# Performance work log

Measured on AMD Instinct MI355X. Metric: run time of the kernel, lower is better.

## Reference

```python
import jax, jax.numpy as jnp
import numpy as np
import math

B, S, HID = 2, 2048, 512
H, HKV, QB, VB = 8, 2, 8, 16
W = 256 // QB            # suffix window size = 32
QKD = W * QB             # unfolded qk dim = 256
TAU = 1.0


def setup_inputs() -> dict:
    key = jax.random.key(0)
    ks = jax.random.split(key, 7)
    return {
        "hidden_states": jax.random.normal(ks[0], (B, S, HID), jnp.float32),
        "Wq": jax.random.normal(ks[1], (H * QB, HID), jnp.float32) * (HID ** -0.5),
        "Wk": jax.random.normal(ks[2], (HKV * QB, HID), jnp.float32) * (HID ** -0.5),
        "Wv": jax.random.normal(ks[3], (HKV * VB, HID), jnp.float32) * (HID ** -0.5),
        "Wo": jax.random.normal(ks[4], (HID, H * VB), jnp.float32) * ((H * VB) ** -0.5),
        "v_emb0": jnp.full((H * VB,), -1e-5, jnp.float32),
        "v_emb1": jnp.full((H * VB,), +1e-5, jnp.float32),
    }


def _forward(hidden_states, Wq, Wk, Wv, Wo, v_emb0, v_emb1):
    b, s, _ = hidden_states.shape
    # bit-quantized (soft) q/k/v projections
    q = jnp.tanh((hidden_states @ Wq.T) / TAU).reshape(b, s, H, QB).transpose(0, 2, 1, 3)      # [B,H,S,QB]
    k = jnp.tanh((hidden_states @ Wk.T) / TAU).reshape(b, s, HKV, QB).transpose(0, 2, 1, 3)    # [B,HKV,S,QB]
    v = jax.nn.sigmoid((hidden_states @ Wv.T) / TAU).reshape(b, s, HKV, VB).transpose(0, 2, 1, 3)
    # suffix shift of values: F.pad(v, (0,0,-1,1)) -> v[t] <- v[t+1], last position zero
    v = jnp.concatenate([v[:, :, 1:], jnp.zeros_like(v[:, :, :1])], axis=2)                    # [B,HKV,S,VB]
    # left-pad seq by W-1 zeros, then unfold sliding windows of length W
    pad = ((0, 0), (0, 0), (W - 1, 0), (0, 0))
    qp, kp = jnp.pad(q, pad), jnp.pad(k, pad)
    win = jnp.arange(s)[:, None] + jnp.arange(W)[None, :]   # [S,W] window indices into padded seq
    qw = qp[:, :, win, :].reshape(b, H, s, QKD)             # concat window positions x bits
    kw = kp[:, :, win, :].reshape(b, HKV, s, QKD)
    # GQA: repeat kv heads
    rep = H // HKV
    kw = jnp.repeat(kw, rep, axis=1)
    vr = jnp.repeat(v, rep, axis=1)
    scale = 1.0 / math.sqrt(QKD) / TAU
    # custom bias r_j / (r_i + 1) under strictly-causal mask (j < i)
    r = jnp.arange(s, dtype=hidden_states.dtype)
    mask = jnp.tril(jnp.ones((s, s), dtype=bool), -1)
    bias = jnp.where(mask, (r[None, :] / (r[:, None] + 1.0)) / TAU, 0.0)
    scores = jnp.einsum('bhqd,bhkd->bhqk', qw, kw) * scale + bias
    neg = jnp.finfo(scores.dtype).min
    scores = jnp.where(mask, scores, neg)
    # stable masked softmax (fully-masked row 0 -> zero weights instead of NaN)
    scores = scores - jax.lax.stop_gradient(jnp.max(scores, axis=-1, keepdims=True))
    e = jnp.exp(scores) * mask
    attn = e / jnp.maximum(jnp.sum(e, axis=-1, keepdims=True), 1e-30)
    out = jnp.einsum('bhqk,bhkd->bhqd', attn, vr)           # [B,H,S,VB]
    out = out.transpose(0, 2, 1, 3).reshape(b, s, H * VB)
    # learned emb0/emb1 interpolation
    out = out * v_emb1 + (1.0 - out) * v_emb0
    return out @ Wo.T


def reference(hidden_states, Wq, Wk, Wv, Wo, v_emb0, v_emb1):
    return _forward(hidden_states, Wq, Wk, Wv, Wo, v_emb0, v_emb1)
```

## Files before the change

### kernel.cpp

```cpp
#include <hip/hip_runtime.h>
#include <hip/hip_bf16.h>

typedef unsigned int u32;
typedef unsigned short u16;
typedef float f32x4 __attribute__((ext_vector_type(4)));
typedef short s16x8 __attribute__((ext_vector_type(8)));
typedef u32 u32x2 __attribute__((ext_vector_type(2)));

#define B_   2
#define S_   2048
#define HID_ 512
#define H_   8
#define HKV_ 2
#define QB_  8
#define VB_  16
#define NQ_  64
#define NC_  112
#define HVB_ 128
#define SCALE_ 0.0625f
#define MFIX_  17.0f

__device__ __forceinline__ u16 f2bf(float f) {
    u32 b = __builtin_bit_cast(u32, f);
    b += 0x7FFFu + ((b >> 16) & 1u);
    return (u16)(b >> 16);
}
__device__ __forceinline__ float bf2f(u16 h) {
    u32 b = ((u32)h) << 16;
    return __builtin_bit_cast(float, b);
}
__device__ __forceinline__ f32x4 mfma16(s16x8 a, s16x8 b, f32x4 c) {
    return __builtin_amdgcn_mfma_f32_16x16x32_bf16(a, b, c, 0, 0, 0);
}
__device__ __forceinline__ float fast_tanh(float x) {
    float e = __expf(2.f * x);
    return 1.f - 2.f * __builtin_amdgcn_rcpf(e + 1.f);
}
__device__ __forceinline__ float fast_sigmoid(float x) {
    return __builtin_amdgcn_rcpf(1.f + __expf(-x));
}

__global__ void k0_convert(const float* __restrict__ Wq, const float* __restrict__ Wk,
                           const float* __restrict__ Wv, const float* __restrict__ Wo,
                           u16* __restrict__ W2c_hi, u16* __restrict__ W2c_lo,
                           u16* __restrict__ W2o_hi, u16* __restrict__ W2o_lo) {
    int idx = blockIdx.x * 256 + threadIdx.x;
    if (idx < NC_ * HID_) {
        int n = idx >> 9, k = idx & 511;
        float v = (n < NQ_) ? Wq[n * HID_ + k]
                : (n < NQ_ + 16) ? Wk[(n - NQ_) * HID_ + k]
                : Wv[(n - NQ_ - 16) * HID_ + k];
        int dst = ((k >> 5) * NC_ + n) * 32 + (k & 31);
        u16 hi = f2bf(v);
        W2c_hi[dst] = hi;
        W2c_lo[dst] = f2bf(v - bf2f(hi));
    }
    if (idx < HID_ * HVB_) {
        int o = idx >> 7, k = idx & 127;
        float v = Wo[idx];
        int dst = ((k >> 5) * HID_ + o) * 32 + (k & 31);
        u16 hi = f2bf(v);
        W2o_hi[dst] = hi;
        W2o_lo[dst] = f2bf(v - bf2f(hi));
    }
}

__global__ __launch_bounds__(256) void k1_proj(
    const float* __restrict__ hidden,
    const u16* __restrict__ W2c_hi, const u16* __restrict__ W2c_lo,
    u16* __restrict__ qb, u16* __restrict__ kb, u16* __restrict__ vt)
{
    __shared__ __align__(16) u32 Ahi[16 * 256];
    __shared__ __align__(16) u32 Alo[16 * 256];
    char* AhiB = (char*)Ahi;
    char* AloB = (char*)Alo;
    const int tid = threadIdx.x;
    const int r0 = blockIdx.x * 16;

    #pragma unroll
    for (int it = 0; it < 8; ++it) {
        int v4 = it * 256 + tid;
        int m = v4 >> 7, c4 = v4 & 127;
        f32x4 x = *(const f32x4*)&hidden[(r0 + m) * HID_ + 4 * c4];
        u16 h0 = f2bf(x[0]), h1 = f2bf(x[1]), h2 = f2bf(x[2]), h3 = f2bf(x[3]);
        u16 l0 = f2bf(x[0] - bf2f(h0)), l1 = f2bf(x[1] - bf2f(h1));
        u16 l2 = f2bf(x[2] - bf2f(h2)), l3 = f2bf(x[3] - bf2f(h3));
        int byt = (c4 * 8) ^ ((m & 7) << 4);
        *(u32x2*)(AhiB + m * 1024 + byt) = (u32x2){(u32)h0 | ((u32)h1 << 16), (u32)h2 | ((u32)h3 << 16)};
        *(u32x2*)(AloB + m * 1024 + byt) = (u32x2){(u32)l0 | ((u32)l1 << 16), (u32)l2 | ((u32)l3 << 16)};
    }
    __syncthreads();

    const int wv = tid >> 6, lane = tid & 63;
    const int li = lane & 15, lo4 = lane >> 4;
    const int nf = (wv == 3) ? 1 : 2;
    const int fl[2] = {wv, wv + 4};

    f32x4 acc[2];
    acc[0] = (f32x4){0.f, 0.f, 0.f, 0.f};
    acc[1] = (f32x4){0.f, 0.f, 0.f, 0.f};

    for (int kc = 0; kc < 16; ++kc) {
        int off = (64 * kc + 16 * lo4) ^ ((li & 7) << 4);
        s16x8 ah = *(const s16x8*)(AhiB + li * 1024 + off);
        s16x8 al = *(const s16x8*)(AloB + li * 1024 + off);
        #pragma unroll
        for (int u = 0; u < 2; ++u) {
            if (u < nf) {
                int n = fl[u] * 16 + li;
                int bidx = (kc * NC_ + n) * 32 + 8 * lo4;
                s16x8 bh = *(const s16x8*)&W2c_hi[bidx];
                s16x8 bl = *(const s16x8*)&W2c_lo[bidx];
                acc[u] = mfma16(ah, bh, acc[u]);
                acc[u] = mfma16(ah, bl, acc[u]);
                acc[u] = mfma16(al, bh, acc[u]);
            }
        }
    }

    #pragma unroll
    for (int u = 0; u < 2; ++u) {
        if (u < nf) {
            int n = fl[u] * 16 + li;
            #pragma unroll
            for (int reg = 0; reg < 4; ++reg) {
                int gs = r0 + 4 * lo4 + reg;
                int b = gs >> 11, s = gs & 2047;
                float pre = acc[u][reg];
                if (n < NQ_) {
                    int h = n >> 3, bit = n & 7;
                    qb[(((b * H_ + h) * S_) + s) * QB_ + bit] = f2bf(fast_tanh(pre));
                } else if (n < NQ_ + 16) {
                    int nk = n - NQ_;
                    kb[(((b * HKV_ + (nk >> 3)) * S_) + s) * QB_ + (nk & 7)] = f2bf(fast_tanh(pre));
                } else {
                    int nv = n - NQ_ - 16;
                    int hv = nv >> 4, vb = nv & 15;
                    u16 sig = f2bf(fast_sigmoid(pre));
                    if (s > 0)
                        vt[((b * HKV_ + hv) * VB_ + vb) * S_ + (s - 1)] = sig;
                    if (s == S_ - 1)
                        vt[((b * HKV_ + hv) * VB_ + vb) * S_ + (S_ - 1)] = 0;
                }
            }
        }
    }
}

__global__ __launch_bounds__(512, 4) void k2_attn(
    const u16* __restrict__ qb, const u16* __restrict__ kb, const u16* __restrict__ vt,
    const float* __restrict__ vemb0, const float* __restrict__ vemb1,
    float* __restrict__ AO)
{
    __shared__ __align__(16) u16 ks[2][2][96 * 8];
    __shared__ __align__(16) u16 psa[8][16 * 72];
    __shared__ __align__(16) float Om[8][16][17];
    __shared__ float lv[8][16];

    const int tid = threadIdx.x;
    const int bid = blockIdx.x;
    const int rb = bid >> 4;
    const int r  = (rb < 16) ? (31 - rb) : (rb - 16);
    const int I0 = r * 64;
    const int nJ = r + 1;
    const int bh = bid & 15;
    const int b = bh >> 3, h = bh & 7, hkv = h >> 2;

    const int qhb = ((b * H_ + h) * S_) * QB_;
    const int khb = ((b * HKV_ + hkv) * S_) * QB_;
    const int vhb = ((b * HKV_ + hkv) * VB_) * S_;

    const int w = tid >> 6, lane = tid & 63;
    const int g = w >> 2, wr = w & 3;
    const int li = lane & 15, lo4 = lane >> 4;
    const int tloc = tid & 255;

    u16* psw = psa[w];

    s16x8 af[8];
    {
        const int gr0 = I0 - 31 + 16 * wr + li + lo4;
        const u16* qp = qb + qhb + gr0 * QB_;
        #pragma unroll
        for (int kk = 0; kk < 8; ++kk) {
            s16x8 v = {0, 0, 0, 0, 0, 0, 0, 0};
            if (gr0 + 4 * kk >= 0) v = *(const s16x8*)(qp + kk * 32);
            af[kk] = v;
        }
    }

    int iv[4];
    float binv[4];
    #pragma unroll
    for (int reg = 0; reg < 4; ++reg) {
        iv[reg] = I0 + 16 * wr + 4 * lo4 + reg;
        binv[reg] = 1.0f / (float)(iv[reg] + 1);
    }

    f32x4 O = (f32x4){0.f, 0.f, 0.f, 0.f};
    float lsum[4] = {0.f, 0.f, 0.f, 0.f};

    const u16* vtp = vt + vhb + li * S_ + 8 * lo4;

    if (g < nJ && tloc < 96) {
        int gr = 64 * g - 31 + tloc;
        s16x8 v = {0, 0, 0, 0, 0, 0, 0, 0};
        if (gr >= 0) v = *(const s16x8*)(kb + khb + gr * QB_);
        *(s16x8*)&ks[g][0][tloc * 8] = v;
    }
    __syncthreads();

    const int nT = (nJ + 1) >> 1;
    for (int t = 0; t < nT; ++t) {
        const int cb = t & 1;
        const int jt = 2 * t + g;

        const bool do_stage = ((jt + 2) < nJ) && (tloc < 96);
        s16x8 stg;
        if (do_stage)
            stg = *(const s16x8*)(kb + khb + (64 * (jt + 2) - 31 + tloc) * QB_);

        if (jt < nJ) {
            const u16* kbuf = &ks[g][cb][(li + lo4) * 8];
            f32x4 sacc[4];
            #pragma unroll
            for (int ns = 0; ns < 4; ++ns) sacc[ns] = (f32x4){0.f, 0.f, 0.f, 0.f};
            #pragma unroll
            for (int m = 0; m < 20; ++m) {
                s16x8 f = *(const s16x8*)(kbuf + 32 * m);
                #pragma unroll
                for (int kk = (m & 3); kk < 8; kk += 4) {
                    int ns = (m - kk) >> 2;
                    if (ns >= 0 && ns < 4)
                        sacc[ns] = mfma16(af[kk], f, sacc[ns]);
                }
            }
            const int J0 = jt * 64;
            int jv[4];
            #pragma unroll
            for (int ns = 0; ns < 4; ++ns) jv[ns] = J0 + 16 * ns + li;
            #pragma unroll
            for (int reg = 0; reg < 4; ++reg) {
                #pragma unroll
                for (int ns = 0; ns < 4; ++ns) {
                    float s = fmaf(sacc[ns][reg], SCALE_, (float)jv[ns] * binv[reg]);
                    float p = (jv[ns] < iv[reg]) ? __expf(s - MFIX_) : 0.0f;
                    lsum[reg] += p;
                    psw[(4 * lo4 + reg) * 72 + 16 * ns + li] = f2bf(p);
                }
            }
            #pragma unroll
            for (int kk2 = 0; kk2 < 2; ++kk2) {
                s16x8 pa = *(const s16x8*)&psw[li * 72 + 32 * kk2 + 8 * lo4];
                s16x8 pb = *(const s16x8*)(vtp + J0 + 32 * kk2);
                O = mfma16(pa, pb, O);
            }
        }

        if (do_stage)
            *(s16x8*)&ks[g][cb ^ 1][tloc * 8] = stg;

        __syncthreads();
    }

    #pragma unroll
    for (int reg = 0; reg < 4; ++reg) {
        float l = lsum[reg];
        l += __shfl_xor(l, 1);
        l += __shfl_xor(l, 2);
        l += __shfl_xor(l, 4);
        l += __shfl_xor(l, 8);
        Om[w][4 * lo4 + reg][li] = O[reg];
        if (li == 0) lv[w][4 * lo4 + reg] = l;
    }
    __syncthreads();

    if (g == 0) {
        const int hc = h * VB_ + li;
        const float e0 = vemb0[hc], e1 = vemb1[hc];
        #pragma unroll
        for (int reg = 0; reg < 4; ++reg) {
            const int row = 4 * lo4 + reg;
            float Oc = Om[w][row][li] + Om[w + 4][row][li];
            float lc = lv[w][row] + lv[w + 4][row];
            float o = Oc / fmaxf(lc, 1e-30f);
            const int s = I0 + 16 * wr + row;
            AO[(b * S_ + s) * HVB_ + hc] = e0 + o * (e1 - e0);
        }
    }
}

__global__ __launch_bounds__(256) void k3_out(
    const float* __restrict__ AO,
    const u16* __restrict__ W2o_hi, const u16* __restrict__ W2o_lo,
    float* __restrict__ out)
{
    __shared__ __align__(16) u32 Ahi[16 * 64];
    __shared__ __align__(16) u32 Alo[16 * 64];
    char* AhiB = (char*)Ahi;
    char* AloB = (char*)Alo;
    const int tid = threadIdx.x;
    const int r0 = blockIdx.x * 16;

    #pragma unroll
    for (int it = 0; it < 2; ++it) {
        int v4 = it * 256 + tid;
        int m = v4 >> 5, c4 = v4 & 31;
        f32x4 x = *(const f32x4*)&AO[(r0 + m) * HVB_ + 4 * c4];
        u16 h0 = f2bf(x[0]), h1 = f2bf(x[1]), h2 = f2bf(x[2]), h3 = f2bf(x[3]);
        u16 l0 = f2bf(x[0] - bf2f(h0)), l1 = f2bf(x[1] - bf2f(h1));
        u16 l2 = f2bf(x[2] - bf2f(h2)), l3 = f2bf(x[3] - bf2f(h3));
        int byt = (c4 * 8) ^ ((m & 7) << 4);
        *(u32x2*)(AhiB + m * 256 + byt) = (u32x2){(u32)h0 | ((u32)h1 << 16), (u32)h2 | ((u32)h3 << 16)};
        *(u32x2*)(AloB + m * 256 + byt) = (u32x2){(u32)l0 | ((u32)l1 << 16), (u32)l2 | ((u32)l3 << 16)};
    }
    __syncthreads();

    const int wv = tid >> 6, lane = tid & 63;
    const int li = lane & 15, lo4 = lane >> 4;

    f32x4 acc[8];
    #pragma unroll
    for (int f = 0; f < 8; ++f) acc[f] = (f32x4){0.f, 0.f, 0.f, 0.f};

    #pragma unroll
    for (int kc = 0; kc < 4; ++kc) {
        int off = (64 * kc + 16 * lo4) ^ ((li & 7) << 4);
        s16x8 ah = *(const s16x8*)(AhiB + li * 256 + off);
        s16x8 al = *(const s16x8*)(AloB + li * 256 + off);
        #pragma unroll
        for (int f = 0; f < 8; ++f) {
            int o = wv * 128 + f * 16 + li;
            int bidx = (kc * HID_ + o) * 32 + 8 * lo4;
            s16x8 bh = *(const s16x8*)&W2o_hi[bidx];
            s16x8 bl = *(const s16x8*)&W2o_lo[bidx];
            acc[f] = mfma16(ah, bh, acc[f]);
            acc[f] = mfma16(ah, bl, acc[f]);
            acc[f] = mfma16(al, bh, acc[f]);
        }
    }

    #pragma unroll
    for (int f = 0; f < 8; ++f) {
        int o = wv * 128 + f * 16 + li;
        #pragma unroll
        for (int reg = 0; reg < 4; ++reg)
            out[(r0 + 4 * lo4 + reg) * HID_ + o] = acc[f][reg];
    }
}

extern "C" void kernel_launch(void* const* d_in, const int* in_sizes, int n_in,
                              void* d_out, int out_size, void* d_ws, size_t ws_size,
                              hipStream_t stream)
{
    (void)in_sizes; (void)n_in; (void)out_size;
    const float* hidden = (const float*)d_in[0];
    const float* Wq = (const float*)d_in[1];
    const float* Wk = (const float*)d_in[2];
    const float* Wv = (const float*)d_in[3];
    const float* Wo = (const float*)d_in[4];
    const float* ve0 = (const float*)d_in[5];
    const float* ve1 = (const float*)d_in[6];
    float* out = (float*)d_out;

    char* base = (char*)d_ws;
    u16* qb    = (u16*)(base);
    u16* kb    = (u16*)(base + 524288);
    u16* vt    = (u16*)(base + 655360);
    float* AO  = (float*)(base + 917504);
    u16* W2c_hi = (u16*)(base + 3014656);
    u16* W2c_lo = (u16*)(base + 3129344);
    u16* W2o_hi = (u16*)(base + 3244032);
    u16* W2o_lo = (u16*)(base + 3375104);
    if (ws_size < 3506176) return;

    hipLaunchKernelGGL(k0_convert, dim3(256), dim3(256), 0, stream,
                       Wq, Wk, Wv, Wo, W2c_hi, W2c_lo, W2o_hi, W2o_lo);
    hipLaunchKernelGGL(k1_proj, dim3(256), dim3(256), 0, stream,
                       hidden, W2c_hi, W2c_lo, qb, kb, vt);
    hipLaunchKernelGGL(k2_attn, dim3(512), dim3(512), 0, stream,
                       qb, kb, vt, ve0, ve1, AO);
    hipLaunchKernelGGL(k3_out, dim3(256), dim3(256), 0, stream,
                       AO, W2o_hi, W2o_lo, out);
}
```

Before: 63.66 us.

## Drop split-bf16 GEMMs, store AO as bf16, restructure attention to 256-thread blocks

```diff
diff --git a/kernel.cpp b/kernel.cpp
--- a/kernel.cpp
+++ b/kernel.cpp
@@ -5,7 +5,6 @@
 typedef unsigned short u16;
 typedef float f32x4 __attribute__((ext_vector_type(4)));
 typedef short s16x8 __attribute__((ext_vector_type(8)));
-typedef u32 u32x2 __attribute__((ext_vector_type(2)));
 
 #define B_   2
 #define S_   2048
@@ -15,7 +14,6 @@
 #define QB_  8
 #define VB_  16
 #define NQ_  64
-#define NC_  112
 #define HVB_ 128
 #define SCALE_ 0.0625f
 #define MFIX_  17.0f
@@ -42,86 +40,51 @@
 
 __global__ void k0_convert(const float* __restrict__ Wq, const float* __restrict__ Wk,
                            const float* __restrict__ Wv, const float* __restrict__ Wo,
-                           u16* __restrict__ W2c_hi, u16* __restrict__ W2c_lo,
-                           u16* __restrict__ W2o_hi, u16* __restrict__ W2o_lo) {
+                           u16* __restrict__ Wc, u16* __restrict__ Wob) {
     int idx = blockIdx.x * 256 + threadIdx.x;
-    if (idx < NC_ * HID_) {
+    {
         int n = idx >> 9, k = idx & 511;
         float v = (n < NQ_) ? Wq[n * HID_ + k]
                 : (n < NQ_ + 16) ? Wk[(n - NQ_) * HID_ + k]
-                : Wv[(n - NQ_ - 16) * HID_ + k];
-        int dst = ((k >> 5) * NC_ + n) * 32 + (k & 31);
-        u16 hi = f2bf(v);
-        W2c_hi[dst] = hi;
-        W2c_lo[dst] = f2bf(v - bf2f(hi));
-    }
-    if (idx < HID_ * HVB_) {
-        int o = idx >> 7, k = idx & 127;
-        float v = Wo[idx];
-        int dst = ((k >> 5) * HID_ + o) * 32 + (k & 31);
-        u16 hi = f2bf(v);
-        W2o_hi[dst] = hi;
-        W2o_lo[dst] = f2bf(v - bf2f(hi));
-    }
+                : (n < 112) ? Wv[(n - NQ_ - 16) * HID_ + k] : 0.f;
+        Wc[idx] = f2bf(v);
+    }
+    Wob[idx] = f2bf(Wo[idx]);
 }
 
 __global__ __launch_bounds__(256) void k1_proj(
-    const float* __restrict__ hidden,
-    const u16* __restrict__ W2c_hi, const u16* __restrict__ W2c_lo,
+    const float* __restrict__ hidden, const u16* __restrict__ Wc,
     u16* __restrict__ qb, u16* __restrict__ kb, u16* __restrict__ vt)
 {
-    __shared__ __align__(16) u32 Ahi[16 * 256];
-    __shared__ __align__(16) u32 Alo[16 * 256];
-    char* AhiB = (char*)Ahi;
-    char* AloB = (char*)Alo;
     const int tid = threadIdx.x;
     const int r0 = blockIdx.x * 16;
-
-    #pragma unroll
-    for (int it = 0; it < 8; ++it) {
-        int v4 = it * 256 + tid;
-        int m = v4 >> 7, c4 = v4 & 127;
-        f32x4 x = *(const f32x4*)&hidden[(r0 + m) * HID_ + 4 * c4];
-        u16 h0 = f2bf(x[0]), h1 = f2bf(x[1]), h2 = f2bf(x[2]), h3 = f2bf(x[3]);
-        u16 l0 = f2bf(x[0] - bf2f(h0)), l1 = f2bf(x[1] - bf2f(h1));
-        u16 l2 = f2bf(x[2] - bf2f(h2)), l3 = f2bf(x[3] - bf2f(h3));
-        int byt = (c4 * 8) ^ ((m & 7) << 4);
-        *(u32x2*)(AhiB + m * 1024 + byt) = (u32x2){(u32)h0 | ((u32)h1 << 16), (u32)h2 | ((u32)h3 << 16)};
-        *(u32x2*)(AloB + m * 1024 + byt) = (u32x2){(u32)l0 | ((u32)l1 << 16), (u32)l2 | ((u32)l3 << 16)};
-    }
-    __syncthreads();
-
     const int wv = tid >> 6, lane = tid & 63;
     const int li = lane & 15, lo4 = lane >> 4;
-    const int nf = (wv == 3) ? 1 : 2;
-    const int fl[2] = {wv, wv + 4};
+
+    const float* hrow = hidden + (r0 + li) * HID_;
 
     f32x4 acc[2];
     acc[0] = (f32x4){0.f, 0.f, 0.f, 0.f};
     acc[1] = (f32x4){0.f, 0.f, 0.f, 0.f};
 
+    #pragma unroll
     for (int kc = 0; kc < 16; ++kc) {
-        int off = (64 * kc + 16 * lo4) ^ ((li & 7) << 4);
-        s16x8 ah = *(const s16x8*)(AhiB + li * 1024 + off);
-        s16x8 al = *(const s16x8*)(AloB + li * 1024 + off);
+        f32x4 x0 = *(const f32x4*)&hrow[32 * kc + 8 * lo4];
+        f32x4 x1 = *(const f32x4*)&hrow[32 * kc + 8 * lo4 + 4];
+        s16x8 a = { (short)f2bf(x0[0]), (short)f2bf(x0[1]), (short)f2bf(x0[2]), (short)f2bf(x0[3]),
+                    (short)f2bf(x1[0]), (short)f2bf(x1[1]), (short)f2bf(x1[2]), (short)f2bf(x1[3]) };
         #pragma unroll
         for (int u = 0; u < 2; ++u) {
-            if (u < nf) {
-                int n = fl[u] * 16 + li;
-                int bidx = (kc * NC_ + n) * 32 + 8 * lo4;
-                s16x8 bh = *(const s16x8*)&W2c_hi[bidx];
-                s16x8 bl = *(const s16x8*)&W2c_lo[bidx];
-                acc[u] = mfma16(ah, bh, acc[u]);
-                acc[u] = mfma16(ah, bl, acc[u]);
-                acc[u] = mfma16(al, bh, acc[u]);
-            }
+            int n = (wv + 4 * u) * 16 + li;
+            s16x8 bfr = *(const s16x8*)&Wc[n * HID_ + 32 * kc + 8 * lo4];
+            acc[u] = mfma16(a, bfr, acc[u]);
         }
     }
 
     #pragma unroll
     for (int u = 0; u < 2; ++u) {
-        if (u < nf) {
-            int n = fl[u] * 16 + li;
+        int n = (wv + 4 * u) * 16 + li;
+        if (n < 112) {
             #pragma unroll
             for (int reg = 0; reg < 4; ++reg) {
                 int gs = r0 + 4 * lo4 + reg;
@@ -147,15 +110,15 @@
     }
 }
 
-__global__ __launch_bounds__(512, 4) void k2_attn(
+__global__ __launch_bounds__(256, 2) void k2_attn(
     const u16* __restrict__ qb, const u16* __restrict__ kb, const u16* __restrict__ vt,
     const float* __restrict__ vemb0, const float* __restrict__ vemb1,
-    float* __restrict__ AO)
+    u16* __restrict__ AO)
 {
     __shared__ __align__(16) u16 ks[2][2][96 * 8];
-    __shared__ __align__(16) u16 psa[8][16 * 72];
-    __shared__ __align__(16) float Om[8][16][17];
-    __shared__ float lv[8][16];
+    __shared__ __align__(16) u16 psa[4][32 * 72];
+    __shared__ __align__(16) float Om[4][2][16][17];
+    __shared__ float lv[4][2][16];
 
     const int tid = threadIdx.x;
     const int bid = blockIdx.x;
@@ -171,38 +134,43 @@
     const int vhb = ((b * HKV_ + hkv) * VB_) * S_;
 
     const int w = tid >> 6, lane = tid & 63;
-    const int g = w >> 2, wr = w & 3;
+    const int rw = w & 1, g = w >> 1;
     const int li = lane & 15, lo4 = lane >> 4;
-    const int tloc = tid & 255;
+    const int tloc = tid & 127;
 
     u16* psw = psa[w];
 
-    s16x8 af[8];
-    {
-        const int gr0 = I0 - 31 + 16 * wr + li + lo4;
+    s16x8 qf[2][8];
+    #pragma unroll
+    for (int ig = 0; ig < 2; ++ig) {
+        const int gr0 = I0 + 32 * rw + 16 * ig + li - 31 + lo4;
         const u16* qp = qb + qhb + gr0 * QB_;
         #pragma unroll
         for (int kk = 0; kk < 8; ++kk) {
             s16x8 v = {0, 0, 0, 0, 0, 0, 0, 0};
             if (gr0 + 4 * kk >= 0) v = *(const s16x8*)(qp + kk * 32);
-            af[kk] = v;
-        }
-    }
-
-    int iv[4];
-    float binv[4];
-    #pragma unroll
-    for (int reg = 0; reg < 4; ++reg) {
-        iv[reg] = I0 + 16 * wr + 4 * lo4 + reg;
-        binv[reg] = 1.0f / (float)(iv[reg] + 1);
-    }
-
-    f32x4 O = (f32x4){0.f, 0.f, 0.f, 0.f};
-    float lsum[4] = {0.f, 0.f, 0.f, 0.f};
+            qf[ig][kk] = v;
+        }
+    }
+
+    float binv[2][4];
+    #pragma unroll
+    for (int ig = 0; ig < 2; ++ig)
+        #pragma unroll
+        for (int reg = 0; reg < 4; ++reg) {
+            float d = (float)(I0 + 32 * rw + 16 * ig + 4 * lo4 + reg + 1);
+            float rc = __builtin_amdgcn_rcpf(d);
+            binv[ig][reg] = rc * (2.f - d * rc);
+        }
+
+    f32x4 O[2];
+    O[0] = (f32x4){0.f, 0.f, 0.f, 0.f};
+    O[1] = (f32x4){0.f, 0.f, 0.f, 0.f};
+    float lsum[2][4] = {{0.f, 0.f, 0.f, 0.f}, {0.f, 0.f, 0.f, 0.f}};
 
     const u16* vtp = vt + vhb + li * S_ + 8 * lo4;
 
-    if (g < nJ && tloc < 96) {
+    if (g < nJ && tloc < 95) {
         int gr = 64 * g - 31 + tloc;
         s16x8 v = {0, 0, 0, 0, 0, 0, 0, 0};
         if (gr >= 0) v = *(const s16x8*)(kb + khb + gr * QB_);
@@ -215,45 +183,66 @@
         const int cb = t & 1;
         const int jt = 2 * t + g;
 
-        const bool do_stage = ((jt + 2) < nJ) && (tloc < 96);
+        const bool do_stage = ((jt + 2) < nJ) && (tloc < 95);
         s16x8 stg;
         if (do_stage)
             stg = *(const s16x8*)(kb + khb + (64 * (jt + 2) - 31 + tloc) * QB_);
 
         if (jt < nJ) {
             const u16* kbuf = &ks[g][cb][(li + lo4) * 8];
-            f32x4 sacc[4];
-            #pragma unroll
-            for (int ns = 0; ns < 4; ++ns) sacc[ns] = (f32x4){0.f, 0.f, 0.f, 0.f};
+            f32x4 sacc[2][4];
+            #pragma unroll
+            for (int ig = 0; ig < 2; ++ig)
+                #pragma unroll
+                for (int ns = 0; ns < 4; ++ns)
+                    sacc[ig][ns] = (f32x4){0.f, 0.f, 0.f, 0.f};
             #pragma unroll
             for (int m = 0; m < 20; ++m) {
                 s16x8 f = *(const s16x8*)(kbuf + 32 * m);
-                #pragma unroll
-                for (int kk = (m & 3); kk < 8; kk += 4) {
-                    int ns = (m - kk) >> 2;
-                    if (ns >= 0 && ns < 4)
-                        sacc[ns] = mfma16(af[kk], f, sacc[ns]);
-                }
-            }
+                {
+                    int kk = m & 3, ns = m >> 2;
+                    if (ns < 4) {
+                        sacc[0][ns] = mfma16(qf[0][kk], f, sacc[0][ns]);
+                        sacc[1][ns] = mfma16(qf[1][kk], f, sacc[1][ns]);
+                    }
+                }
+                {
+                    int kk = (m & 3) + 4, ns = (m >> 2) - 1;
+                    if (ns >= 0) {
+                        sacc[0][ns] = mfma16(qf[0][kk], f, sacc[0][ns]);
+                        sacc[1][ns] = mfma16(qf[1][kk], f, sacc[1][ns]);
+                    }
+                }
+            }
+
             const int J0 = jt * 64;
             int jv[4];
             #pragma unroll
             for (int ns = 0; ns < 4; ++ns) jv[ns] = J0 + 16 * ns + li;
             #pragma unroll
-            for (int reg = 0; reg < 4; ++reg) {
+            for (int ig = 0; ig < 2; ++ig) {
                 #pragma unroll
-                for (int ns = 0; ns < 4; ++ns) {
-                    float s = fmaf(sacc[ns][reg], SCALE_, (float)jv[ns] * binv[reg]);
-                    float p = (jv[ns] < iv[reg]) ? __expf(s - MFIX_) : 0.0f;
-                    lsum[reg] += p;
-                    psw[(4 * lo4 + reg) * 72 + 16 * ns + li] = f2bf(p);
-                }
-            }
-            #pragma unroll
-            for (int kk2 = 0; kk2 < 2; ++kk2) {
-                s16x8 pa = *(const s16x8*)&psw[li * 72 + 32 * kk2 + 8 * lo4];
-                s16x8 pb = *(const s16x8*)(vtp + J0 + 32 * kk2);
-                O = mfma16(pa, pb, O);
+                for (int reg = 0; reg < 4; ++reg) {
+                    const int i = I0 + 32 * rw + 16 * ig + 4 * lo4 + reg;
+                    const float bi = binv[ig][reg];
+                    #pragma unroll
+                    for (int ns = 0; ns < 4; ++ns) {
+                        float s = fmaf(sacc[ig][ns][reg], SCALE_, (float)jv[ns] * bi);
+                        float p = (jv[ns] < i) ? __expf(s - MFIX_) : 0.0f;
+                        lsum[ig][reg] += p;
+                        psw[(ig * 16 + 4 * lo4 + reg) * 72 + 16 * ns + li] = f2bf(p);
+                    }
+                }
+            }
+
+            #pragma unroll
+            for (int ig = 0; ig < 2; ++ig) {
+                #pragma unroll
+                for (int kk2 = 0; kk2 < 2; ++kk2) {
+                    s16x8 pa = *(const s16x8*)&psw[(ig * 16 + li) * 72 + 32 * kk2 + 8 * lo4];
+                    s16x8 pb = *(const s16x8*)(vtp + J0 + 32 * kk2);
+                    O[ig] = mfma16(pa, pb, O[ig]);
+                }
             }
         }
 
@@ -264,14 +253,17 @@
     }
 
     #pragma unroll
-    for (int reg = 0; reg < 4; ++reg) {
-        float l = lsum[reg];
-        l += __shfl_xor(l, 1);
-        l += __shfl_xor(l, 2);
-        l += __shfl_xor(l, 4);
-        l += __shfl_xor(l, 8);
-        Om[w][4 * lo4 + reg][li] = O[reg];
-        if (li == 0) lv[w][4 * lo4 + reg] = l;
+    for (int ig = 0; ig < 2; ++ig) {
+        #pragma unroll
+        for (int reg = 0; reg < 4; ++reg) {
+            float l = lsum[ig][reg];
+            l += __shfl_xor(l, 1);
+            l += __shfl_xor(l, 2);
+            l += __shfl_xor(l, 4);
+            l += __shfl_xor(l, 8);
+            Om[w][ig][4 * lo4 + reg][li] = O[ig][reg];
+            if (li == 0) lv[w][ig][4 * lo4 + reg] = l;
+        }
     }
     __syncthreads();
 
@@ -279,73 +271,56 @@
         const int hc = h * VB_ + li;
         const float e0 = vemb0[hc], e1 = vemb1[hc];
         #pragma unroll
-        for (int reg = 0; reg < 4; ++reg) {
-            const int row = 4 * lo4 + reg;
-            float Oc = Om[w][row][li] + Om[w + 4][row][li];
-            float lc = lv[w][row] + lv[w + 4][row];
-            float o = Oc / fmaxf(lc, 1e-30f);
-            const int s = I0 + 16 * wr + row;
-            AO[(b * S_ + s) * HVB_ + hc] = e0 + o * (e1 - e0);
+        for (int ig = 0; ig < 2; ++ig) {
+            #pragma unroll
+            for (int reg = 0; reg < 4; ++reg) {
+                const int row = 4 * lo4 + reg;
+                float Oc = Om[w][ig][row][li] + Om[w + 2][ig][row][li];
+                float lc = lv[w][ig][row] + lv[w + 2][ig][row];
+                float lr = fmaxf(lc, 1e-30f);
+                float rinv = __builtin_amdgcn_rcpf(lr);
+                rinv = rinv * (2.f - lr * rinv);
+                float o = Oc * rinv;
+                const int s = I0 + 32 * rw + 16 * ig + row;
+                AO[(b * S_ + s) * HVB_ + hc] = f2bf(e0 + o * (e1 - e0));
+            }
         }
     }
 }
 
 __global__ __launch_bounds__(256) void k3_out(
-    const float* __restrict__ AO,
-    const u16* __restrict__ W2o_hi, const u16* __restrict__ W2o_lo,
+    const u16* __restrict__ AO, const u16* __restrict__ Wob,
     float* __restrict__ out)
 {
-    __shared__ __align__(16) u32 Ahi[16 * 64];
-    __shared__ __align__(16) u32 Alo[16 * 64];
-    char* AhiB = (char*)Ahi;
-    char* AloB = (char*)Alo;
     const int tid = threadIdx.x;
-    const int r0 = blockIdx.x * 16;
-
-    #pragma unroll
-    for (int it = 0; it < 2; ++it) {
-        int v4 = it * 256 + tid;
-        int m = v4 >> 5, c4 = v4 & 31;
-        f32x4 x = *(const f32x4*)&AO[(r0 + m) * HVB_ + 4 * c4];
-        u16 h0 = f2bf(x[0]), h1 = f2bf(x[1]), h2 = f2bf(x[2]), h3 = f2bf(x[3]);
-        u16 l0 = f2bf(x[0] - bf2f(h0)), l1 = f2bf(x[1] - bf2f(h1));
-        u16 l2 = f2bf(x[2] - bf2f(h2)), l3 = f2bf(x[3] - bf2f(h3));
-        int byt = (c4 * 8) ^ ((m & 7) << 4);
-        *(u32x2*)(AhiB + m * 256 + byt) = (u32x2){(u32)h0 | ((u32)h1 << 16), (u32)h2 | ((u32)h3 << 16)};
-        *(u32x2*)(AloB + m * 256 + byt) = (u32x2){(u32)l0 | ((u32)l1 << 16), (u32)l2 | ((u32)l3 << 16)};
-    }
-    __syncthreads();
-
+    const int r0 = (blockIdx.x >> 2) * 16;
+    const int cg = blockIdx.x & 3;
     const int wv = tid >> 6, lane = tid & 63;
     const int li = lane & 15, lo4 = lane >> 4;
 
-    f32x4 acc[8];
-    #pragma unroll
-    for (int f = 0; f < 8; ++f) acc[f] = (f32x4){0.f, 0.f, 0.f, 0.f};
+    const u16* arow = AO + (r0 + li) * HVB_;
+
+    f32x4 acc[2];
+    acc[0] = (f32x4){0.f, 0.f, 0.f, 0.f};
+    acc[1] = (f32x4){0.f, 0.f, 0.f, 0.f};
 
     #pragma unroll
     for (int kc = 0; kc < 4; ++kc) {
-        int off = (64 * kc + 16 * lo4) ^ ((li & 7) << 4);
-        s16x8 ah = *(const s16x8*)(AhiB + li * 256 + off);
-        s16x8 al = *(const s16x8*)(AloB + li * 256 + off);
-        #pragma unroll
-        for (int f = 0; f < 8; ++f) {
-            int o = wv * 128 + f * 16 + li;
-            int bidx = (kc * HID_ + o) * 32 + 8 * lo4;
-            s16x8 bh = *(const s16x8*)&W2o_hi[bidx];
-            s16x8 bl = *(const s16x8*)&W2o_lo[bidx];
-            acc[f] = mfma16(ah, bh, acc[f]);
-            acc[f] = mfma16(ah, bl, acc[f]);
-            acc[f] = mfma16(al, bh, acc[f]);
-        }
-    }
-
-    #pragma unroll
-    for (int f = 0; f < 8; ++f) {
-        int o = wv * 128 + f * 16 + li;
+        s16x8 a = *(const s16x8*)&arow[32 * kc + 8 * lo4];
+        #pragma unroll
+        for (int u = 0; u < 2; ++u) {
+            int o = cg * 128 + (wv + 4 * u) * 16 + li;
+            s16x8 bfr = *(const s16x8*)&Wob[o * HVB_ + 32 * kc + 8 * lo4];
+            acc[u] = mfma16(a, bfr, acc[u]);
+        }
+    }
+
+    #pragma unroll
+    for (int u = 0; u < 2; ++u) {
+        int o = cg * 128 + (wv + 4 * u) * 16 + li;
         #pragma unroll
         for (int reg = 0; reg < 4; ++reg)
-            out[(r0 + 4 * lo4 + reg) * HID_ + o] = acc[f][reg];
+            out[(r0 + 4 * lo4 + reg) * HID_ + o] = acc[u][reg];
     }
 }
 
@@ -364,22 +339,20 @@
     float* out = (float*)d_out;
 
     char* base = (char*)d_ws;
-    u16* qb    = (u16*)(base);
-    u16* kb    = (u16*)(base + 524288);
-    u16* vt    = (u16*)(base + 655360);
-    float* AO  = (float*)(base + 917504);
-    u16* W2c_hi = (u16*)(base + 3014656);
-    u16* W2c_lo = (u16*)(base + 3129344);
-    u16* W2o_hi = (u16*)(base + 3244032);
-    u16* W2o_lo = (u16*)(base + 3375104);
-    if (ws_size < 3506176) return;
+    u16* qb  = (u16*)(base);
+    u16* kb  = (u16*)(base + 524288);
+    u16* vt  = (u16*)(base + 655360);
+    u16* AO  = (u16*)(base + 917504);
+    u16* Wc  = (u16*)(base + 1966080);
+    u16* Wob = (u16*)(base + 2097152);
+    if (ws_size < 2228224) return;
 
     hipLaunchKernelGGL(k0_convert, dim3(256), dim3(256), 0, stream,
-                       Wq, Wk, Wv, Wo, W2c_hi, W2c_lo, W2o_hi, W2o_lo);
+                       Wq, Wk, Wv, Wo, Wc, Wob);
     hipLaunchKernelGGL(k1_proj, dim3(256), dim3(256), 0, stream,
-                       hidden, W2c_hi, W2c_lo, qb, kb, vt);
-    hipLaunchKernelGGL(k2_attn, dim3(512), dim3(512), 0, stream,
+                       hidden, Wc, qb, kb, vt);
+    hipLaunchKernelGGL(k2_attn, dim3(512), dim3(256), 0, stream,
                        qb, kb, vt, ve0, ve1, AO);
-    hipLaunchKernelGGL(k3_out, dim3(256), dim3(256), 0, stream,
-                       AO, W2o_hi, W2o_lo, out);
-}
+    hipLaunchKernelGGL(k3_out, dim3(1024), dim3(256), 0, stream,
+                       AO, Wob, out);
+}
```

After: 68.83 us. +8.1%, slower.
